# Kernel optimization log

Measured on AMD Instinct MI355X. Metric: run time of the kernel, lower is better.

The kernel has to match this reference:

```python
import jax, jax.numpy as jnp
import numpy as np

EMB_DIM = 1024
N_HEADS = 16
HEAD_DIM = EMB_DIM // N_HEADS


def setup_inputs() -> dict:
    key = jax.random.key(0)
    ks = jax.random.split(key, 6)
    B, T, C = 2, 2048, EMB_DIM
    s = 1.0 / np.sqrt(C)
    return {
        "x": jax.random.normal(ks[0], (B, T, C), dtype=jnp.float32),
        "W_query": jax.random.normal(ks[1], (C, C), dtype=jnp.float32) * s,
        "W_key": jax.random.normal(ks[2], (C, C), dtype=jnp.float32) * s,
        "W_value": jax.random.normal(ks[3], (C, C), dtype=jnp.float32) * s,
        "W_out": jax.random.normal(ks[4], (C, C), dtype=jnp.float32) * s,
        "b_out": jax.random.normal(ks[5], (C,), dtype=jnp.float32) * 0.01,
    }


def reference(x, W_query, W_key, W_value, W_out, b_out):
    # x: [B, T, C]. Linear weights stored as [in, out] (transposed torch layout).
    B, T, C = x.shape
    H, D = N_HEADS, HEAD_DIM

    def split_heads(t):  # [B,T,C] -> [B,H,T,D]
        return t.reshape(B, T, H, D).transpose(0, 2, 1, 3)

    q = split_heads(x @ W_query)
    k = split_heads(x @ W_key)
    v = split_heads(x @ W_value)

    scale = 1.0 / jnp.sqrt(jnp.asarray(D, dtype=x.dtype))
    att = jnp.einsum("bhqd,bhkd->bhqk", q, k) * scale  # [B,H,T,T]
    causal = jnp.tril(jnp.ones((T, T), dtype=bool))
    att = jnp.where(causal[None, None], att, jnp.asarray(-jnp.inf, dtype=att.dtype))
    att = jax.nn.softmax(att, axis=-1)
    # dropout is identity in eval / drop_rate=0
    y = jnp.einsum("bhqk,bhkd->bhqd", att, v)  # [B,H,T,D]
    y = y.transpose(0, 2, 1, 3).reshape(B, T, C)
    return y @ W_out + b_out
```

## Files before the change

kernel.cpp:

```cpp
#include <hip/hip_runtime.h>
#include <hip/hip_bf16.h>
#include <math.h>

#define Bsz 2
#define Tsz 2048
#define Csz 1024
#define Hsz 16
#define Dsz 64

typedef __attribute__((ext_vector_type(8))) short frag8;
typedef __attribute__((ext_vector_type(4))) float f4;
typedef __attribute__((ext_vector_type(8))) unsigned short us8;
typedef __attribute__((ext_vector_type(4))) _Float16 frag4h;
typedef __attribute__((ext_vector_type(8))) _Float16 frag8h;

#if __has_builtin(__builtin_amdgcn_mfma_f32_16x16x16f16)
#define PV_DIRECT 1
#endif

static __device__ __forceinline__ unsigned short f2bf(float f) {
  union { __hip_bfloat16 h; unsigned short u; } c;
  c.h = __float2bfloat16(f);
  return c.u;
}
static __device__ __forceinline__ unsigned short f2h(float f) {
  union { _Float16 h; unsigned short u; } c;
  c.h = (_Float16)f;
  return c.u;
}

#define GLDS16(g, l)                                                        \
  __builtin_amdgcn_global_load_lds(                                         \
      (const __attribute__((address_space(1))) void*)(g),                   \
      (__attribute__((address_space(3))) void*)(l), 16, 0, 0)

#define QSCALE 0.18033688f

__global__ __launch_bounds__(256) void cast_x(const float* __restrict__ x,
                                              unsigned short* __restrict__ xb) {
  const int i = (blockIdx.x * 256 + threadIdx.x) * 8;
  const float4 a = *(const float4*)(x + i);
  const float4 b = *(const float4*)(x + i + 4);
  us8 v;
  v[0] = f2bf(a.x); v[1] = f2bf(a.y); v[2] = f2bf(a.z); v[3] = f2bf(a.w);
  v[4] = f2bf(b.x); v[5] = f2bf(b.y); v[6] = f2bf(b.z); v[7] = f2bf(b.w);
  *(us8*)(xb + i) = v;
}

__global__ __launch_bounds__(256) void transpose_cast(
    const float* __restrict__ s0, const float* __restrict__ s1,
    const float* __restrict__ s2, const float* __restrict__ s3,
    unsigned short* __restrict__ d0, unsigned short* __restrict__ d1,
    unsigned short* __restrict__ d2, unsigned short* __restrict__ d3) {
  __shared__ float Ls[64][65];
  const int mat = blockIdx.x >> 8;
  const int tile = blockIdx.x & 255;
  const float* src = mat == 0 ? s0 : mat == 1 ? s1 : mat == 2 ? s2 : s3;
  unsigned short* dst = mat == 0 ? d0 : mat == 1 ? d1 : mat == 2 ? d2 : d3;
  const int tr0 = (tile >> 4) << 6, tc0 = (tile & 15) << 6;
  const int t = threadIdx.x;
  const int lr = t >> 4, lc = (t & 15) << 2;
#pragma unroll
  for (int j = 0; j < 4; ++j) {
    const float4 v = *(const float4*)(src + (size_t)(tr0 + lr + j * 16) * 1024 + tc0 + lc);
    Ls[lr + j * 16][lc + 0] = v.x;
    Ls[lr + j * 16][lc + 1] = v.y;
    Ls[lr + j * 16][lc + 2] = v.z;
    Ls[lr + j * 16][lc + 3] = v.w;
  }
  __syncthreads();
#pragma unroll
  for (int j = 0; j < 4; ++j) {
    ushort4 v;
    v.x = f2bf(Ls[lc + 0][lr + j * 16]);
    v.y = f2bf(Ls[lc + 1][lr + j * 16]);
    v.z = f2bf(Ls[lc + 2][lr + j * 16]);
    v.w = f2bf(Ls[lc + 3][lr + j * 16]);
    *(ushort4*)(dst + (size_t)(tc0 + lr + j * 16) * 1024 + tr0 + lc) = v;
  }
}

template <int MODE, int MT>
__global__ __launch_bounds__(256) void mm_bt(
    const unsigned short* __restrict__ A, const unsigned short* __restrict__ Bt,
    const float* __restrict__ bias, unsigned short* __restrict__ O0,
    unsigned short* __restrict__ O1, unsigned short* __restrict__ O2,
    float* __restrict__ Of) {
  __shared__ __align__(16) unsigned short As[MT * 32 * 64];
  __shared__ __align__(16) unsigned short Bs[128 * 64];
  const int K = 1024;
  const int tid = threadIdx.x;
  const int wave = tid >> 6, lane = tid & 63;
  const int quad = lane >> 4, l16 = lane & 15;
  const int wrow = (wave >> 1) * (MT * 16), wn = wave & 1;
  const int row0 = blockIdx.y * (MT * 32), col0 = blockIdx.x << 7;

  const int sr = lane >> 3, sg = lane & 7;
  const int g0 = sg ^ sr;
  const unsigned short* gA = A + (size_t)(row0 + wave * (MT * 8) + sr) * K + (g0 << 3);
  const unsigned short* gB = Bt + (size_t)(col0 + wave * 32 + sr) * K + (g0 << 3);

  f4 acc[MT][4];
#pragma unroll
  for (int i = 0; i < MT; ++i)
#pragma unroll
    for (int j = 0; j < 4; ++j) acc[i][j] = (f4){0.f, 0.f, 0.f, 0.f};

  for (int kk = 0; kk < K; kk += 64) {
    __syncthreads();
#pragma unroll
    for (int s = 0; s < MT; ++s)
      GLDS16(gA + kk + (size_t)(s * 8) * K, &As[(wave * (MT * 8) + s * 8) * 64]);
#pragma unroll
    for (int s = 0; s < 4; ++s)
      GLDS16(gB + kk + (size_t)(s * 8) * K, &Bs[(wave * 32 + s * 8) * 64]);
    __syncthreads();

#pragma unroll
    for (int ks = 0; ks < 2; ++ks) {
      frag8 af[MT], bf[4];
#pragma unroll
      for (int mt = 0; mt < MT; ++mt) {
        const int r = wrow + mt * 16 + l16;
        af[mt] = *(const frag8*)&As[r * 64 + (((ks * 4 + quad) ^ (l16 & 7)) << 3)];
      }
#pragma unroll
      for (int nt = 0; nt < 4; ++nt) {
        const int n = wn * 64 + nt * 16 + l16;
        bf[nt] = *(const frag8*)&Bs[n * 64 + (((ks * 4 + quad) ^ (l16 & 7)) << 3)];
      }
#pragma unroll
      for (int mt = 0; mt < MT; ++mt)
#pragma unroll
        for (int nt = 0; nt < 4; ++nt)
          acc[mt][nt] = __builtin_amdgcn_mfma_f32_16x16x32_bf16(af[mt], bf[nt], acc[mt][nt], 0, 0, 0);
    }
  }

  if (MODE == 0) {
    if (col0 < 2048) {
      const bool isK = (col0 >= 1024);
      unsigned short* dst = isK ? O1 : O0;
      const float sc = isK ? 1.0f : QSCALE;
#pragma unroll
      for (int mt = 0; mt < MT; ++mt)
#pragma unroll
        for (int nt = 0; nt < 4; ++nt) {
          const int m = row0 + wrow + mt * 16 + quad * 4;
          const int n = (col0 & 1023) + wn * 64 + nt * 16 + l16;
          const int b = m >> 11, h = n >> 6, d = n & 63;
#pragma unroll
          for (int r = 0; r < 4; ++r) {
            const int tk = (m + r) & (Tsz - 1);
            dst[(((size_t)b * Hsz + h) * Tsz + tk) * Dsz + d] = f2bf(acc[mt][nt][r] * sc);
          }
        }
    } else {
#pragma unroll
      for (int mt = 0; mt < MT; ++mt)
#pragma unroll
        for (int nt = 0; nt < 4; ++nt) {
          const int tok = row0 + wrow + mt * 16 + quad * 4;
          const int ch = (col0 - 2048) + wn * 64 + nt * 16 + l16;
          const int b = tok >> 11, tk = tok & (Tsz - 1);
          const int h = ch >> 6, d = ch & 63;
          ushort4 v;
          v.x = f2h(acc[mt][nt][0]); v.y = f2h(acc[mt][nt][1]);
          v.z = f2h(acc[mt][nt][2]); v.w = f2h(acc[mt][nt][3]);
          *(ushort4*)&O2[(((size_t)b * Hsz + h) * Dsz + d) * Tsz + tk] = v;
        }
    }
  } else {
#pragma unroll
    for (int mt = 0; mt < MT; ++mt)
#pragma unroll
      for (int nt = 0; nt < 4; ++nt) {
        const int m = row0 + wrow + mt * 16 + quad * 4;
        const int n = col0 + wn * 64 + nt * 16 + l16;
        const float bv = bias[n];
#pragma unroll
        for (int r = 0; r < 4; ++r)
          Of[(size_t)(m + r) * Csz + n] = acc[mt][nt][r] + bv;
      }
  }
}

__global__ __launch_bounds__(256, 2) void attn_mfma(
    const unsigned short* __restrict__ Qb,
    const unsigned short* __restrict__ Kb,
    const unsigned short* __restrict__ VTb,
    unsigned short* __restrict__ Y) {
  __shared__ __align__(16) unsigned short Ks[2][2048];
  __shared__ __align__(16) unsigned short Vs[2][2048];
#ifndef PV_DIRECT
  __shared__ __align__(16) unsigned short Pb[4][32 * 72];
#endif
  const int tid = threadIdx.x;
  const int wave = tid >> 6, lane = tid & 63;
  const int quad = lane >> 4, l16 = lane & 15;

  const int bh = blockIdx.x >> 4;
  const int qtr = blockIdx.x & 15;
  const int qt = (bh < 16) ? (15 - qtr) : qtr;
  const int qb0 = qt << 7;
  const int qb_w = qb0 + wave * 32;

  const unsigned short* Qh = Qb + (size_t)bh * Tsz * Dsz;
  const unsigned short* Kh = Kb + (size_t)bh * Tsz * Dsz;
  const unsigned short* Vh = VTb + (size_t)bh * Dsz * Tsz;

  const int kkey = tid >> 3, kc = tid & 7;
  const int vd = tid >> 2, vc = tid & 3;
  const unsigned short* gK = Kh + (size_t)kkey * Dsz + ((kc ^ (kkey & 7)) << 3);
  const unsigned short* gV = Vh + (size_t)vd * Tsz + ((vc ^ ((vd + (vd >> 2)) & 3)) << 3);

  frag8 qf[2][2];
#pragma unroll
  for (int m = 0; m < 2; ++m)
#pragma unroll
    for (int ks = 0; ks < 2; ++ks)
      qf[m][ks] = *(const frag8*)(Qh + (size_t)(qb_w + m * 16 + l16) * Dsz + ks * 32 + quad * 8);

  f4 o[2][4];
  float lsum[2] = {0.f, 0.f};
#pragma unroll
  for (int m = 0; m < 2; ++m)
#pragma unroll
    for (int nt = 0; nt < 4; ++nt) o[m][nt] = (f4){0.f, 0.f, 0.f, 0.f};

  const f4 zf = (f4){0.f, 0.f, 0.f, 0.f};
  const int fl = (l16 + (l16 >> 2)) & 3;
  const int kend_w = qb_w + 32;
  const int nch = (qb0 >> 5) + 4;

  GLDS16(gK, &Ks[0][wave * 512]);
  GLDS16(gV, &Vs[0][wave * 512]);
  GLDS16(gK + (size_t)32 * Dsz, &Ks[1][wave * 512]);
  GLDS16(gV + 32, &Vs[1][wave * 512]);
  __syncthreads();

  for (int i = 0; i < nch; ++i) {
    const int k0 = i << 5;
    const int bsel = i & 1;
    if (k0 < kend_w) {
      frag8 kf[2][2];
#pragma unroll
      for (int n = 0; n < 2; ++n)
#pragma unroll
        for (int ks = 0; ks < 2; ++ks)
          kf[n][ks] = *(const frag8*)&Ks[bsel][(n * 16 + l16) * 64 + (((ks * 4 + quad) ^ (l16 & 7)) << 3)];

      f4 st[2][2];
#pragma unroll
      for (int n = 0; n < 2; ++n)
#pragma unroll
        for (int m = 0; m < 2; ++m) {
          f4 a = __builtin_amdgcn_mfma_f32_16x16x32_bf16(kf[n][0], qf[m][0], zf, 0, 0, 0);
          st[n][m] = __builtin_amdgcn_mfma_f32_16x16x32_bf16(kf[n][1], qf[m][1], a, 0, 0, 0);
        }

      const bool domask = (k0 + 31 > qb_w);
      frag4h paf[2][2];
#pragma unroll
      for (int m = 0; m < 2; ++m) {
        const int qv = qb_w + m * 16 + l16;
#pragma unroll
        for (int n = 0; n < 2; ++n) {
          const int key0 = k0 + n * 16 + quad * 4;
          float p[4];
#pragma unroll
          for (int r = 0; r < 4; ++r) {
            float sv = st[n][m][r];
            if (domask && (key0 + r > qv)) sv = -INFINITY;
            p[r] = __builtin_amdgcn_exp2f(sv);
          }
          lsum[m] += (p[0] + p[1]) + (p[2] + p[3]);
          frag4h ph;
          ph[0] = (_Float16)p[0]; ph[1] = (_Float16)p[1];
          ph[2] = (_Float16)p[2]; ph[3] = (_Float16)p[3];
          paf[m][n] = ph;
        }
      }

#ifdef PV_DIRECT
      frag4h vf[2][4];
#pragma unroll
      for (int n = 0; n < 2; ++n)
#pragma unroll
        for (int nt = 0; nt < 4; ++nt) {
          const int g = 2 * n + (quad >> 1);
          vf[n][nt] = *(const frag4h*)&Vs[bsel][(nt * 16 + l16) * 32 + ((g ^ fl) << 3) + ((quad & 1) << 2)];
        }
#pragma unroll
      for (int m = 0; m < 2; ++m)
#pragma unroll
        for (int nt = 0; nt < 4; ++nt) {
          f4 a = __builtin_amdgcn_mfma_f32_16x16x16f16(paf[m][0], vf[0][nt], o[m][nt], 0, 0, 0);
          o[m][nt] = __builtin_amdgcn_mfma_f32_16x16x16f16(paf[m][1], vf[1][nt], a, 0, 0, 0);
        }
#else
      unsigned short* Pw = &Pb[wave][0];
#pragma unroll
      for (int m = 0; m < 2; ++m)
#pragma unroll
        for (int n = 0; n < 2; ++n)
          *(frag4h*)&Pw[(m * 16 + l16) * 72 + n * 16 + quad * 4] = paf[m][n];
      frag8h pfh[2];
#pragma unroll
      for (int m = 0; m < 2; ++m)
        pfh[m] = *(const frag8h*)&Pw[(m * 16 + l16) * 72 + quad * 8];
      frag8h vf8[4];
#pragma unroll
      for (int nt = 0; nt < 4; ++nt)
        vf8[nt] = *(const frag8h*)&Vs[bsel][(nt * 16 + l16) * 32 + ((quad ^ fl) << 3)];
#pragma unroll
      for (int m = 0; m < 2; ++m)
#pragma unroll
        for (int nt = 0; nt < 4; ++nt)
          o[m][nt] = __builtin_amdgcn_mfma_f32_16x16x32_f16(pfh[m], vf8[nt], o[m][nt], 0, 0, 0);
#endif
    }
    __syncthreads();
    if (i + 2 < nch) {
      GLDS16(gK + (size_t)(k0 + 64) * Dsz, &Ks[bsel][wave * 512]);
      GLDS16(gV + (k0 + 64), &Vs[bsel][wave * 512]);
    }
  }

#pragma unroll
  for (int m = 0; m < 2; ++m) {
    lsum[m] += __shfl_xor(lsum[m], 16);
    lsum[m] += __shfl_xor(lsum[m], 32);
  }

  const int b = bh >> 4, h = bh & 15;
#pragma unroll
  for (int m = 0; m < 2; ++m)
#pragma unroll
    for (int r = 0; r < 4; ++r) {
      const float inv = 1.f / __shfl(lsum[m], quad * 4 + r);
      const int t = qb_w + m * 16 + quad * 4 + r;
      unsigned short* yp = Y + ((size_t)b * Tsz + t) * Csz + h * 64 + l16;
#pragma unroll
      for (int nt = 0; nt < 4; ++nt)
        yp[nt * 16] = f2bf(o[m][nt][r] * inv);
    }
}

extern "C" void kernel_launch(void* const* d_in, const int* in_sizes, int n_in,
                              void* d_out, int out_size, void* d_ws, size_t ws_size,
                              hipStream_t stream) {
  const float* x  = (const float*)d_in[0];
  const float* Wq = (const float*)d_in[1];
  const float* Wk = (const float*)d_in[2];
  const float* Wv = (const float*)d_in[3];
  const float* Wo = (const float*)d_in[4];
  const float* bo = (const float*)d_in[5];

  const size_t NEL = (size_t)Bsz * Tsz * Csz;
  const size_t WSZ = (size_t)Csz * Csz;
  unsigned short* xb  = (unsigned short*)d_ws;
  unsigned short* WT  = xb + NEL;
  unsigned short* WoT = WT + 3 * WSZ;
  unsigned short* Qb  = WoT + WSZ;
  unsigned short* Kb  = Qb + NEL;
  unsigned short* VTb = Kb + NEL;
  unsigned short* Yb  = VTb + NEL;

  cast_x<<<NEL / 2048, 256, 0, stream>>>(x, xb);
  transpose_cast<<<1024, 256, 0, stream>>>(Wq, Wk, Wv, Wo,
                                           WT, WT + WSZ, WT + 2 * WSZ, WoT);

  mm_bt<0, 4><<<dim3(24, 32), 256, 0, stream>>>(xb, WT, nullptr, Qb, Kb, VTb, nullptr);

  attn_mfma<<<Bsz * Hsz * (Tsz / 128), 256, 0, stream>>>(Qb, Kb, VTb, Yb);

  mm_bt<2, 2><<<dim3(8, 64), 256, 0, stream>>>(Yb, WoT, bo, nullptr, nullptr, nullptr,
                                               (float*)d_out);
}
```

Baseline: 199.3 us.

## Drop LDS staging in attention; load K/V fragments directly from global memory

The attention kernel no longer stages K and V tiles in LDS with async global_load_lds and block barriers. Each wave now independently owns a 32-query tile, loads K and V fragments straight from global memory (relying on L2/cache reuse), and runs with no __syncthreads. The V^T projection epilogue now writes tokens in a permuted order inside each 32-token chunk, so one 16-byte load per lane yields both halves of the PV MFMA operands. Launch bounds are raised to 4 blocks per SM, and the grid is reordered so the longest causal rows are scheduled first. In exchange, K/V reuse across the four waves of a block is lost, so global and L2 traffic per block rises.

```diff
diff --git a/kernel.cpp b/kernel.cpp
--- a/kernel.cpp
+++ b/kernel.cpp
@@ -13,10 +13,6 @@
 typedef __attribute__((ext_vector_type(8))) unsigned short us8;
 typedef __attribute__((ext_vector_type(4))) _Float16 frag4h;
 typedef __attribute__((ext_vector_type(8))) _Float16 frag8h;
-
-#if __has_builtin(__builtin_amdgcn_mfma_f32_16x16x16f16)
-#define PV_DIRECT 1
-#endif
 
 static __device__ __forceinline__ unsigned short f2bf(float f) {
   union { __hip_bfloat16 h; unsigned short u; } c;
@@ -164,10 +160,12 @@
           const int ch = (col0 - 2048) + wn * 64 + nt * 16 + l16;
           const int b = tok >> 11, tk = tok & (Tsz - 1);
           const int h = ch >> 6, d = ch & 63;
+          const int t5 = tk & 31;
+          const int pos = (tk & ~31) + ((t5 >> 4) << 2) + (((t5 >> 2) & 3) << 3) + (t5 & 3);
           ushort4 v;
           v.x = f2h(acc[mt][nt][0]); v.y = f2h(acc[mt][nt][1]);
           v.z = f2h(acc[mt][nt][2]); v.w = f2h(acc[mt][nt][3]);
-          *(ushort4*)&O2[(((size_t)b * Hsz + h) * Dsz + d) * Tsz + tk] = v;
+          *(ushort4*)&O2[(((size_t)b * Hsz + h) * Dsz + d) * Tsz + pos] = v;
         }
     }
   } else {
@@ -185,41 +183,30 @@
   }
 }
 
-__global__ __launch_bounds__(256, 2) void attn_mfma(
+__global__ __launch_bounds__(256, 4) void attn_mfma(
     const unsigned short* __restrict__ Qb,
     const unsigned short* __restrict__ Kb,
     const unsigned short* __restrict__ VTb,
     unsigned short* __restrict__ Y) {
-  __shared__ __align__(16) unsigned short Ks[2][2048];
-  __shared__ __align__(16) unsigned short Vs[2][2048];
-#ifndef PV_DIRECT
-  __shared__ __align__(16) unsigned short Pb[4][32 * 72];
-#endif
-  const int tid = threadIdx.x;
-  const int wave = tid >> 6, lane = tid & 63;
+  const int wave = threadIdx.x >> 6;
+  const int lane = threadIdx.x & 63;
   const int quad = lane >> 4, l16 = lane & 15;
 
-  const int bh = blockIdx.x >> 4;
-  const int qtr = blockIdx.x & 15;
-  const int qt = (bh < 16) ? (15 - qtr) : qtr;
-  const int qb0 = qt << 7;
-  const int qb_w = qb0 + wave * 32;
+  const int jg = blockIdx.x >> 5;
+  const int bh = blockIdx.x & 31;
+  const int j = 63 - 4 * jg - wave;
+  const int qb = j << 5;
 
   const unsigned short* Qh = Qb + (size_t)bh * Tsz * Dsz;
   const unsigned short* Kh = Kb + (size_t)bh * Tsz * Dsz;
-  const unsigned short* Vh = VTb + (size_t)bh * Dsz * Tsz;
-
-  const int kkey = tid >> 3, kc = tid & 7;
-  const int vd = tid >> 2, vc = tid & 3;
-  const unsigned short* gK = Kh + (size_t)kkey * Dsz + ((kc ^ (kkey & 7)) << 3);
-  const unsigned short* gV = Vh + (size_t)vd * Tsz + ((vc ^ ((vd + (vd >> 2)) & 3)) << 3);
+  const _Float16* Vh = (const _Float16*)(VTb + (size_t)bh * Dsz * Tsz);
 
   frag8 qf[2][2];
 #pragma unroll
   for (int m = 0; m < 2; ++m)
 #pragma unroll
     for (int ks = 0; ks < 2; ++ks)
-      qf[m][ks] = *(const frag8*)(Qh + (size_t)(qb_w + m * 16 + l16) * Dsz + ks * 32 + quad * 8);
+      qf[m][ks] = *(const frag8*)(Qh + (size_t)(qb + m * 16 + l16) * Dsz + ks * 32 + quad * 8);
 
   f4 o[2][4];
   float lsum[2] = {0.f, 0.f};
@@ -227,104 +214,62 @@
   for (int m = 0; m < 2; ++m)
 #pragma unroll
     for (int nt = 0; nt < 4; ++nt) o[m][nt] = (f4){0.f, 0.f, 0.f, 0.f};
-
   const f4 zf = (f4){0.f, 0.f, 0.f, 0.f};
-  const int fl = (l16 + (l16 >> 2)) & 3;
-  const int kend_w = qb_w + 32;
-  const int nch = (qb0 >> 5) + 4;
-
-  GLDS16(gK, &Ks[0][wave * 512]);
-  GLDS16(gV, &Vs[0][wave * 512]);
-  GLDS16(gK + (size_t)32 * Dsz, &Ks[1][wave * 512]);
-  GLDS16(gV + 32, &Vs[1][wave * 512]);
-  __syncthreads();
-
-  for (int i = 0; i < nch; ++i) {
-    const int k0 = i << 5;
-    const int bsel = i & 1;
-    if (k0 < kend_w) {
-      frag8 kf[2][2];
-#pragma unroll
-      for (int n = 0; n < 2; ++n)
-#pragma unroll
-        for (int ks = 0; ks < 2; ++ks)
-          kf[n][ks] = *(const frag8*)&Ks[bsel][(n * 16 + l16) * 64 + (((ks * 4 + quad) ^ (l16 & 7)) << 3)];
-
-      f4 st[2][2];
-#pragma unroll
-      for (int n = 0; n < 2; ++n)
-#pragma unroll
-        for (int m = 0; m < 2; ++m) {
-          f4 a = __builtin_amdgcn_mfma_f32_16x16x32_bf16(kf[n][0], qf[m][0], zf, 0, 0, 0);
-          st[n][m] = __builtin_amdgcn_mfma_f32_16x16x32_bf16(kf[n][1], qf[m][1], a, 0, 0, 0);
+
+  for (int c = 0; c <= j; ++c) {
+    const int k0 = c << 5;
+    frag8 kf[2][2];
+#pragma unroll
+    for (int n = 0; n < 2; ++n)
+#pragma unroll
+      for (int ks = 0; ks < 2; ++ks)
+        kf[n][ks] = *(const frag8*)(Kh + (size_t)(k0 + n * 16 + l16) * Dsz + ks * 32 + quad * 8);
+    frag8h vf[4];
+#pragma unroll
+    for (int nt = 0; nt < 4; ++nt)
+      vf[nt] = *(const frag8h*)(Vh + (size_t)(nt * 16 + l16) * Tsz + k0 + quad * 8);
+
+    f4 st[2][2];
+#pragma unroll
+    for (int n = 0; n < 2; ++n)
+#pragma unroll
+      for (int m = 0; m < 2; ++m) {
+        f4 a = __builtin_amdgcn_mfma_f32_16x16x32_bf16(kf[n][0], qf[m][0], zf, 0, 0, 0);
+        st[n][m] = __builtin_amdgcn_mfma_f32_16x16x32_bf16(kf[n][1], qf[m][1], a, 0, 0, 0);
+      }
+
+    const bool dm = (c == j);
+    frag4h paf[2][2];
+#pragma unroll
+    for (int m = 0; m < 2; ++m) {
+      const int qq = m * 16 + l16;
+#pragma unroll
+      for (int n = 0; n < 2; ++n) {
+        const int key0 = n * 16 + quad * 4;
+        float p[4];
+#pragma unroll
+        for (int r = 0; r < 4; ++r) {
+          float sv = st[n][m][r];
+          if (dm && (key0 + r > qq)) sv = -INFINITY;
+          p[r] = __builtin_amdgcn_exp2f(sv);
         }
-
-      const bool domask = (k0 + 31 > qb_w);
-      frag4h paf[2][2];
-#pragma unroll
-      for (int m = 0; m < 2; ++m) {
-        const int qv = qb_w + m * 16 + l16;
-#pragma unroll
-        for (int n = 0; n < 2; ++n) {
-          const int key0 = k0 + n * 16 + quad * 4;
-          float p[4];
-#pragma unroll
-          for (int r = 0; r < 4; ++r) {
-            float sv = st[n][m][r];
-            if (domask && (key0 + r > qv)) sv = -INFINITY;
-            p[r] = __builtin_amdgcn_exp2f(sv);
-          }
-          lsum[m] += (p[0] + p[1]) + (p[2] + p[3]);
-          frag4h ph;
-          ph[0] = (_Float16)p[0]; ph[1] = (_Float16)p[1];
-          ph[2] = (_Float16)p[2]; ph[3] = (_Float16)p[3];
-          paf[m][n] = ph;
-        }
-      }
-
-#ifdef PV_DIRECT
-      frag4h vf[2][4];
-#pragma unroll
-      for (int n = 0; n < 2; ++n)
-#pragma unroll
-        for (int nt = 0; nt < 4; ++nt) {
-          const int g = 2 * n + (quad >> 1);
-          vf[n][nt] = *(const frag4h*)&Vs[bsel][(nt * 16 + l16) * 32 + ((g ^ fl) << 3) + ((quad & 1) << 2)];
-        }
-#pragma unroll
-      for (int m = 0; m < 2; ++m)
-#pragma unroll
-        for (int nt = 0; nt < 4; ++nt) {
-          f4 a = __builtin_amdgcn_mfma_f32_16x16x16f16(paf[m][0], vf[0][nt], o[m][nt], 0, 0, 0);
-          o[m][nt] = __builtin_amdgcn_mfma_f32_16x16x16f16(paf[m][1], vf[1][nt], a, 0, 0, 0);
-        }
-#else
-      unsigned short* Pw = &Pb[wave][0];
-#pragma unroll
-      for (int m = 0; m < 2; ++m)
-#pragma unroll
-        for (int n = 0; n < 2; ++n)
-          *(frag4h*)&Pw[(m * 16 + l16) * 72 + n * 16 + quad * 4] = paf[m][n];
-      frag8h pfh[2];
-#pragma unroll
-      for (int m = 0; m < 2; ++m)
-        pfh[m] = *(const frag8h*)&Pw[(m * 16 + l16) * 72 + quad * 8];
-      frag8h vf8[4];
-#pragma unroll
-      for (int nt = 0; nt < 4; ++nt)
-        vf8[nt] = *(const frag8h*)&Vs[bsel][(nt * 16 + l16) * 32 + ((quad ^ fl) << 3)];
-#pragma unroll
-      for (int m = 0; m < 2; ++m)
-#pragma unroll
-        for (int nt = 0; nt < 4; ++nt)
-          o[m][nt] = __builtin_amdgcn_mfma_f32_16x16x32_f16(pfh[m], vf8[nt], o[m][nt], 0, 0, 0);
-#endif
+        lsum[m] += (p[0] + p[1]) + (p[2] + p[3]);
+        frag4h ph;
+        ph[0] = (_Float16)p[0]; ph[1] = (_Float16)p[1];
+        ph[2] = (_Float16)p[2]; ph[3] = (_Float16)p[3];
+        paf[m][n] = ph;
+      }
     }
-    __syncthreads();
-    if (i + 2 < nch) {
-      GLDS16(gK + (size_t)(k0 + 64) * Dsz, &Ks[bsel][wave * 512]);
-      GLDS16(gV + (k0 + 64), &Vs[bsel][wave * 512]);
-    }
+
+#pragma unroll
+    for (int m = 0; m < 2; ++m)
+#pragma unroll
+      for (int nt = 0; nt < 4; ++nt) {
+        const frag4h vlo = __builtin_shufflevector(vf[nt], vf[nt], 0, 1, 2, 3);
+        const frag4h vhi = __builtin_shufflevector(vf[nt], vf[nt], 4, 5, 6, 7);
+        f4 a = __builtin_amdgcn_mfma_f32_16x16x16f16(paf[m][0], vlo, o[m][nt], 0, 0, 0);
+        o[m][nt] = __builtin_amdgcn_mfma_f32_16x16x16f16(paf[m][1], vhi, a, 0, 0, 0);
+      }
   }
 
 #pragma unroll
@@ -339,7 +284,7 @@
 #pragma unroll
     for (int r = 0; r < 4; ++r) {
       const float inv = 1.f / __shfl(lsum[m], quad * 4 + r);
-      const int t = qb_w + m * 16 + quad * 4 + r;
+      const int t = qb + m * 16 + quad * 4 + r;
       unsigned short* yp = Y + ((size_t)b * Tsz + t) * Csz + h * 64 + l16;
 #pragma unroll
       for (int nt = 0; nt < 4; ++nt)
@@ -373,7 +318,7 @@
 
   mm_bt<0, 4><<<dim3(24, 32), 256, 0, stream>>>(xb, WT, nullptr, Qb, Kb, VTb, nullptr);
 
-  attn_mfma<<<Bsz * Hsz * (Tsz / 128), 256, 0, stream>>>(Qb, Kb, VTb, Yb);
+  attn_mfma<<<512, 256, 0, stream>>>(Qb, Kb, VTb, Yb);
 
   mm_bt<2, 2><<<dim3(8, 64), 256, 0, stream>>>(Yb, WoT, bo, nullptr, nullptr, nullptr,
                                                (float*)d_out);
```

After: 227.4 us. 14.1% more time.
